# Kernel tuning notes

Hardware: AMD Instinct MI355X
Metric: run time of the kernel (lower is better)

The kernel has to match this reference:

```python
import jax, jax.numpy as jnp
import numpy as np

B, T, V, E, H, D = 2, 2048, 32000, 1024, 16, 64


def setup_inputs() -> dict:
    key = jax.random.key(0)
    ks = jax.random.split(key, 8)
    s = 0.02  # init scale
    return {
        "X": jax.random.randint(ks[0], (B, T), 0, V),
        "tok_emb": jax.random.normal(ks[1], (V, E), jnp.float32) * s,
        "pos_emb": jax.random.normal(ks[2], (T, E), jnp.float32) * s,
        "Wq": jax.random.normal(ks[3], (H, E, D), jnp.float32) * s,
        "Wk": jax.random.normal(ks[4], (H, E, D), jnp.float32) * s,
        "Wv": jax.random.normal(ks[5], (H, E, D), jnp.float32) * s,
        "lm_W": jax.random.normal(ks[6], (E, V), jnp.float32) * s,
        "lm_b": jnp.zeros((V,), jnp.float32),
    }


def reference(X, tok_emb, pos_emb, Wq, Wk, Wv, lm_W, lm_b):
    b, t = X.shape
    d = Wq.shape[-1]
    # token + position embedding
    x = tok_emb[X] + pos_emb[:t]  # [B,T,E]
    # per-head projections (stacked heads)
    q = jnp.einsum("bte,hed->bhtd", x, Wq)
    k = jnp.einsum("bte,hed->bhtd", x, Wk)
    v = jnp.einsum("bte,hed->bhtd", x, Wv)
    # causal attention, scale = head_size**-0.5
    scores = jnp.einsum("bhtd,bhsd->bhts", q, k) * (d ** -0.5)  # [B,H,T,T]
    mask = jnp.tril(jnp.ones((t, t), bool))
    scores = jnp.where(mask, scores, -jnp.inf)
    wei = jax.nn.softmax(scores, axis=-1)
    out = jnp.einsum("bhts,bhsd->bhtd", wei, v)
    out = out.transpose(0, 2, 1, 3).reshape(b, t, -1)  # concat heads -> [B,T,H*D]
    logits = out @ lm_W + lm_b  # [B,T,V]
    return logits
```

## Files before the change

kernel.cpp:

```cpp
#include <hip/hip_runtime.h>
#include <hip/hip_bf16.h>
#include <cstdint>

#define TSEQ 2048
#define NB   2
#define NH   16
#define EDIM 1024
#define DDIM 64
#define VOC  32000
#define MROWS (NB*TSEQ)
#define QKVN  (3*EDIM)

typedef _Float16 f16x8 __attribute__((ext_vector_type(8)));
typedef float    f32x4 __attribute__((ext_vector_type(4)));
typedef unsigned short u16x4v __attribute__((ext_vector_type(4)));
typedef unsigned short u16x8v __attribute__((ext_vector_type(8)));

__device__ __forceinline__ unsigned short f2h_bits(float v) {
  return __builtin_bit_cast(unsigned short, (_Float16)v);
}

__device__ __forceinline__ void gload_lds16(const void* g, void* l) {
  __builtin_amdgcn_global_load_lds((__attribute__((address_space(1))) void*)(g),
                                   (__attribute__((address_space(3))) void*)(l),
                                   16, 0, 0);
}

__global__ __launch_bounds__(256) void embed_kernel(
    const int* __restrict__ X, const float* __restrict__ tokE,
    const float* __restrict__ posE, unsigned short* __restrict__ x) {
  int g = blockIdx.x * 256 + threadIdx.x;
  int row = g >> 7;
  int e8  = (g & 127) * 8;
  int tk  = X[row];
  int tp  = row & (TSEQ - 1);
  const float4* ta = reinterpret_cast<const float4*>(&tokE[(size_t)tk * EDIM + e8]);
  const float4* pa = reinterpret_cast<const float4*>(&posE[(size_t)tp * EDIM + e8]);
  float4 a0 = ta[0], a1 = ta[1], p0 = pa[0], p1 = pa[1];
  u16x8v o;
  o[0] = f2h_bits(a0.x + p0.x); o[1] = f2h_bits(a0.y + p0.y);
  o[2] = f2h_bits(a0.z + p0.z); o[3] = f2h_bits(a0.w + p0.w);
  o[4] = f2h_bits(a1.x + p1.x); o[5] = f2h_bits(a1.y + p1.y);
  o[6] = f2h_bits(a1.z + p1.z); o[7] = f2h_bits(a1.w + p1.w);
  *reinterpret_cast<u16x8v*>(&x[(size_t)row * EDIM + e8]) = o;
}

__global__ __launch_bounds__(256) void trans_qkvw(
    const float* __restrict__ Wq, const float* __restrict__ Wk,
    const float* __restrict__ Wv, unsigned short* __restrict__ Wt) {
  __shared__ float ts[64][65];
  int bid = blockIdx.x;
  int mat = bid >> 8;
  int h   = (bid >> 4) & 15;
  int et  = bid & 15;
  const float* src = (mat == 0 ? Wq : (mat == 1 ? Wk : Wv)) + (size_t)h * EDIM * DDIM;
  int t = threadIdx.x;
  int rr = t >> 4, c4 = (t & 15) * 4;
#pragma unroll
  for (int p = 0; p < 4; ++p) {
    int r = p * 16 + rr;
    float4 v = *reinterpret_cast<const float4*>(&src[(size_t)(et * 64 + r) * DDIM + c4]);
    ts[r][c4 + 0] = v.x; ts[r][c4 + 1] = v.y; ts[r][c4 + 2] = v.z; ts[r][c4 + 3] = v.w;
  }
  __syncthreads();
#pragma unroll
  for (int p = 0; p < 4; ++p) {
    int dr = p * 16 + rr;
    u16x4v o;
#pragma unroll
    for (int j = 0; j < 4; ++j) o[j] = f2h_bits(ts[c4 + j][dr]);
    *reinterpret_cast<u16x4v*>(&Wt[((size_t)(mat * EDIM + h * 64 + dr)) * EDIM + et * 64 + c4]) = o;
  }
}

__global__ __launch_bounds__(256) void trans_lmw(
    const float* __restrict__ W, unsigned short* __restrict__ Wt) {
  __shared__ float ts[64][65];
  int bid = blockIdx.x;
  int vt = bid / 16, et = bid % 16;
  int t = threadIdx.x;
  int rr = t >> 4, c4 = (t & 15) * 4;
#pragma unroll
  for (int p = 0; p < 4; ++p) {
    int r = p * 16 + rr;
    float4 v = *reinterpret_cast<const float4*>(&W[(size_t)(et * 64 + r) * VOC + vt * 64 + c4]);
    ts[r][c4 + 0] = v.x; ts[r][c4 + 1] = v.y; ts[r][c4 + 2] = v.z; ts[r][c4 + 3] = v.w;
  }
  __syncthreads();
#pragma unroll
  for (int p = 0; p < 4; ++p) {
    int vr = p * 16 + rr;
    u16x4v o;
#pragma unroll
    for (int j = 0; j < 4; ++j) o[j] = f2h_bits(ts[c4 + j][vr]);
    *reinterpret_cast<u16x4v*>(&Wt[(size_t)(vt * 64 + vr) * EDIM + et * 64 + c4]) = o;
  }
}

template <bool F32OUT, bool BIAS>
__global__ __launch_bounds__(512, 4) void gemm128(
    const unsigned short* __restrict__ A, const unsigned short* __restrict__ Bt,
    float* __restrict__ Cf, unsigned short* __restrict__ Ch,
    const float* __restrict__ bias, int N, int K) {
  __shared__ __align__(16) unsigned short lds[3 * 12288];
  const int tid = threadIdx.x;
  const int w = tid >> 6, l = tid & 63;
  const int wr = w >> 2, wc = w & 3;
  const int l15 = l & 15, lhi = l >> 4;
  const int orig = blockIdx.x;
  const int bx = orig >> 5;
  const int by = orig & 31;
  const int m0 = by * 128, n0 = bx * 256;
  const int swzc = lhi ^ ((l15 >> 1) & 3);
  const int aOff = (wr * 64 + l15) * 32 + swzc * 8;
  const int bOff = 4096 + (wc * 64 + l15) * 32 + swzc * 8;
  const int sr = l >> 2;
  const int sc = (l & 3) ^ ((l >> 3) & 3);
  const unsigned short* PA = A  + (size_t)(m0 + w * 16 + sr) * K + sc * 8;
  const unsigned short* PB = Bt + (size_t)(n0 + w * 16 + sr) * K + sc * 8;
  const int dOff = w * 512;

#define STAGE32(ts, slot) do {                                                \
    gload_lds16(PA + (size_t)(ts) * 32, &lds[(slot) * 12288 + dOff]);         \
    gload_lds16(PB + (size_t)(ts) * 32, &lds[(slot) * 12288 + 4096 + dOff]);  \
    gload_lds16(PB + (size_t)128 * K + (size_t)(ts) * 32,                     \
                &lds[(slot) * 12288 + 8192 + dOff]);                          \
  } while (0)

  f32x4 acc[4][4] = {};
  STAGE32(0, 0);
  STAGE32(1, 1);
  asm volatile("s_waitcnt vmcnt(3)" ::: "memory");
  __builtin_amdgcn_sched_barrier(0);
  __builtin_amdgcn_s_barrier();

  const int NT = K >> 5;
  int slotC = 0;
  for (int t = 0; t < NT; ++t) {
    const int base = slotC * 12288;
    const int ts = (t + 2 < NT) ? (t + 2) : (NT - 1);
    int dslot = slotC + 2; if (dslot >= 3) dslot -= 3;
    STAGE32(ts, dslot);
    f16x8 bf[4];
#pragma unroll
    for (int q = 0; q < 4; ++q) bf[q] = *reinterpret_cast<const f16x8*>(&lds[base + bOff + q * 512]);
    f16x8 afq = *reinterpret_cast<const f16x8*>(&lds[base + aOff]);
    __builtin_amdgcn_s_setprio(1);
#pragma unroll
    for (int mi = 0; mi < 4; ++mi) {
      f16x8 afn = *reinterpret_cast<const f16x8*>(&lds[base + aOff + (((mi + 1) & 3)) * 512]);
#pragma unroll
      for (int ni = 0; ni < 4; ++ni)
        acc[mi][ni] = __builtin_amdgcn_mfma_f32_16x16x32_f16(afq, bf[ni], acc[mi][ni], 0, 0, 0);
      afq = afn;
    }
    __builtin_amdgcn_s_setprio(0);
    asm volatile("s_waitcnt vmcnt(3)" ::: "memory");
    __builtin_amdgcn_sched_barrier(0);
    __builtin_amdgcn_s_barrier();
    ++slotC; if (slotC == 3) slotC = 0;
  }
#undef STAGE32
  asm volatile("s_waitcnt vmcnt(0)" ::: "memory");

#pragma unroll
  for (int ni = 0; ni < 4; ++ni) {
    const int col = n0 + wc * 64 + ni * 16 + l15;
    float bv = BIAS ? bias[col] : 0.0f;
#pragma unroll
    for (int mi = 0; mi < 4; ++mi) {
#pragma unroll
      for (int r = 0; r < 4; ++r) {
        const size_t row = (size_t)m0 + wr * 64 + mi * 16 + lhi * 4 + r;
        float v = acc[mi][ni][r] + bv;
        if constexpr (F32OUT) __builtin_nontemporal_store(v, &Cf[row * (size_t)N + col]);
        else                  Ch[row * (size_t)N + col] = f2h_bits(v);
      }
    }
  }
}

template <bool F32OUT, bool BIAS>
__global__ __launch_bounds__(256, 2) void gemm128w(
    const unsigned short* __restrict__ A, const unsigned short* __restrict__ Bt,
    float* __restrict__ Cf, unsigned short* __restrict__ Ch,
    const float* __restrict__ bias, int N, int K) {
  __shared__ __align__(16) unsigned short lds[3 * 12288];
  const int tid = threadIdx.x;
  const int w = tid >> 6, l = tid & 63;
  const int l15 = l & 15, lhi = l >> 4;
  const int orig = blockIdx.x;
  const int bx = orig >> 5;
  const int by = orig & 31;
  const int m0 = by * 128, n0 = bx * 256;

  const int swzc = lhi ^ ((l15 >> 1) & 3);
  const int aOff = l15 * 32 + swzc * 8;
  const int bOff = 4096 + (w * 64 + l15) * 32 + swzc * 8;

  const int sr = l >> 2;
  const int sc = (l & 3) ^ ((l >> 3) & 3);
  const unsigned short* PA = A  + (size_t)(m0 + w * 16 + sr) * K + sc * 8;
  const unsigned short* PB = Bt + (size_t)(n0 + w * 64 + sr) * K + sc * 8;

#define STAGEW(ts, slot) do {                                                      \
    gload_lds16(PA + (size_t)(ts) * 32, &lds[(slot) * 12288 + w * 512]);           \
    gload_lds16(PA + (size_t)64 * K + (size_t)(ts) * 32,                           \
                &lds[(slot) * 12288 + 2048 + w * 512]);                            \
    gload_lds16(PB + (size_t)(ts) * 32,                                            \
                &lds[(slot) * 12288 + 4096 + w * 2048]);                           \
    gload_lds16(PB + (size_t)16 * K + (size_t)(ts) * 32,                           \
                &lds[(slot) * 12288 + 4096 + w * 2048 + 512]);                     \
    gload_lds16(PB + (size_t)32 * K + (size_t)(ts) * 32,                           \
                &lds[(slot) * 12288 + 4096 + w * 2048 + 1024]);                    \
    gload_lds16(PB + (size_t)48 * K + (size_t)(ts) * 32,                           \
                &lds[(slot) * 12288 + 4096 + w * 2048 + 1536]);                    \
  } while (0)

  f32x4 acc[8][4] = {};
  STAGEW(0, 0);
  STAGEW(1, 1);
  asm volatile("s_waitcnt vmcnt(6)" ::: "memory");
  __builtin_amdgcn_sched_barrier(0);
  __builtin_amdgcn_s_barrier();

  const int NT = K >> 5;
  int slotC = 0;
  for (int t = 0; t < NT; ++t) {
    const int base = slotC * 12288;
    const int ts = (t + 2 < NT) ? (t + 2) : (NT - 1);
    int dslot = slotC + 2; if (dslot >= 3) dslot -= 3;
    STAGEW(ts, dslot);
    f16x8 bf[4];
#pragma unroll
    for (int q = 0; q < 4; ++q) bf[q] = *reinterpret_cast<const f16x8*>(&lds[base + bOff + q * 512]);
    f16x8 afq = *reinterpret_cast<const f16x8*>(&lds[base + aOff]);
    __builtin_amdgcn_s_setprio(1);
#pragma unroll
    for (int mi = 0; mi < 8; ++mi) {
      f16x8 afn = *reinterpret_cast<const f16x8*>(&lds[base + aOff + (((mi + 1) & 7)) * 512]);
#pragma unroll
      for (int ni = 0; ni < 4; ++ni)
        acc[mi][ni] = __builtin_amdgcn_mfma_f32_16x16x32_f16(afq, bf[ni], acc[mi][ni], 0, 0, 0);
      afq = afn;
    }
    __builtin_amdgcn_s_setprio(0);
    asm volatile("s_waitcnt vmcnt(6)" ::: "memory");
    __builtin_amdgcn_sched_barrier(0);
    __builtin_amdgcn_s_barrier();
    ++slotC; if (slotC == 3) slotC = 0;
  }
#undef STAGEW
  asm volatile("s_waitcnt vmcnt(0)" ::: "memory");

#pragma unroll
  for (int ni = 0; ni < 4; ++ni) {
    const int col = n0 + w * 64 + ni * 16 + l15;
    float bv = BIAS ? bias[col] : 0.0f;
#pragma unroll
    for (int mi = 0; mi < 8; ++mi) {
#pragma unroll
      for (int r = 0; r < 4; ++r) {
        const size_t row = (size_t)m0 + mi * 16 + lhi * 4 + r;
        float v = acc[mi][ni][r] + bv;
        if constexpr (F32OUT) __builtin_nontemporal_store(v, &Cf[row * (size_t)N + col]);
        else                  Ch[row * (size_t)N + col] = f2h_bits(v);
      }
    }
  }
}

__global__ __launch_bounds__(256) void attn_kernel(
    const unsigned short* __restrict__ qkv, unsigned short* __restrict__ out) {
  __shared__ unsigned short Vt[2][64 * 72];
  __shared__ unsigned short Pl[4 * 16 * 72];
  const int bid = blockIdx.x;
  const int qt = bid & 31, bh = bid >> 5;
  const int b = bh >> 4, h = bh & 15;
  const int tid = threadIdx.x, w = tid >> 6, l = tid & 63;
  const int l15 = l & 15, lhi = l >> 4;
  const int q0 = qt * 64;
  const size_t RS = QKVN;
  const unsigned short* qbase = qkv + (size_t)b * TSEQ * RS + h * 64;
  const unsigned short* kbase = qbase + EDIM;
  const unsigned short* vbase = qbase + 2 * EDIM;

  f16x8 qa[2];
  {
    const int qrow = q0 + w * 16 + l15;
#pragma unroll
    for (int ks = 0; ks < 2; ++ks)
      qa[ks] = *reinterpret_cast<const f16x8*>(qbase + (size_t)qrow * RS + ks * 32 + lhi * 8);
  }
  const int vr_ = tid >> 3, vc8 = (tid & 7) * 8;
  {
#pragma unroll
    for (int p = 0; p < 2; ++p) {
      const int rr = vr_ + p * 32;
      u16x8v v = *reinterpret_cast<const u16x8v*>(vbase + (size_t)rr * RS + vc8);
#pragma unroll
      for (int j = 0; j < 8; ++j) Vt[0][(vc8 + j) * 72 + rr] = v[j];
    }
  }
  float m_run[4], l_run[4];
  f32x4 o[4] = {};
#pragma unroll
  for (int r = 0; r < 4; ++r) { m_run[r] = -__builtin_inff(); l_run[r] = 0.f; }
  const int myrow = q0 + w * 16 + lhi * 4;
  unsigned short* pl = &Pl[w * 16 * 72];
  __syncthreads();

  for (int kt = 0; kt <= qt; ++kt) {
    const int kv0 = kt * 64;
    const int tn = (kt + 1 <= qt) ? (kt + 1) : qt;
    u16x8v vpre[2];
#pragma unroll
    for (int p = 0; p < 2; ++p)
      vpre[p] = *reinterpret_cast<const u16x8v*>(
          vbase + (size_t)(tn * 64 + vr_ + p * 32) * RS + vc8);
    f32x4 s[4];
    __builtin_amdgcn_s_setprio(1);
#pragma unroll
    for (int ct = 0; ct < 4; ++ct) {
      f32x4 acc = {};
#pragma unroll
      for (int ks = 0; ks < 2; ++ks) {
        f16x8 kb = *reinterpret_cast<const f16x8*>(
            kbase + (size_t)(kv0 + ct * 16 + l15) * RS + ks * 32 + lhi * 8);
        acc = __builtin_amdgcn_mfma_f32_16x16x32_f16(qa[ks], kb, acc, 0, 0, 0);
      }
      s[ct] = acc;
    }
    __builtin_amdgcn_s_setprio(0);
    if (kt == qt) {
#pragma unroll
      for (int ct = 0; ct < 4; ++ct) {
        const int col = kv0 + ct * 16 + l15;
#pragma unroll
        for (int r = 0; r < 4; ++r) {
          float v = s[ct][r] * 0.125f;
          if (col > myrow + r) v = -__builtin_inff();
          s[ct][r] = v;
        }
      }
    } else {
#pragma unroll
      for (int ct = 0; ct < 4; ++ct)
#pragma unroll
        for (int r = 0; r < 4; ++r) s[ct][r] *= 0.125f;
    }
    float alpha[4];
#pragma unroll
    for (int r = 0; r < 4; ++r) {
      float mx = fmaxf(fmaxf(s[0][r], s[1][r]), fmaxf(s[2][r], s[3][r]));
      mx = fmaxf(mx, __shfl_xor(mx, 1)); mx = fmaxf(mx, __shfl_xor(mx, 2));
      mx = fmaxf(mx, __shfl_xor(mx, 4)); mx = fmaxf(mx, __shfl_xor(mx, 8));
      const float mn = fmaxf(m_run[r], mx);
      alpha[r] = __expf(m_run[r] - mn);
      m_run[r] = mn;
    }
    float rs[4] = {0.f, 0.f, 0.f, 0.f};
#pragma unroll
    for (int ct = 0; ct < 4; ++ct)
#pragma unroll
      for (int r = 0; r < 4; ++r) {
        const float p = __expf(s[ct][r] - m_run[r]);
        s[ct][r] = p;
        rs[r] += p;
      }
#pragma unroll
    for (int r = 0; r < 4; ++r) {
      float t = rs[r];
      t += __shfl_xor(t, 1); t += __shfl_xor(t, 2);
      t += __shfl_xor(t, 4); t += __shfl_xor(t, 8);
      l_run[r] = l_run[r] * alpha[r] + t;
    }
#pragma unroll
    for (int ct = 0; ct < 4; ++ct)
#pragma unroll
      for (int r = 0; r < 4; ++r) o[ct][r] *= alpha[r];
#pragma unroll
    for (int ct = 0; ct < 4; ++ct)
#pragma unroll
      for (int r = 0; r < 4; ++r)
        pl[(lhi * 4 + r) * 72 + ct * 16 + l15] = f2h_bits(s[ct][r]);
    const unsigned short* vt = Vt[kt & 1];
#pragma unroll
    for (int ks = 0; ks < 2; ++ks) {
      f16x8 pa = *reinterpret_cast<const f16x8*>(&pl[l15 * 72 + ks * 32 + lhi * 8]);
      __builtin_amdgcn_s_setprio(1);
#pragma unroll
      for (int ct = 0; ct < 4; ++ct) {
        f16x8 vb = *reinterpret_cast<const f16x8*>(&vt[(ct * 16 + l15) * 72 + ks * 32 + lhi * 8]);
        o[ct] = __builtin_amdgcn_mfma_f32_16x16x32_f16(pa, vb, o[ct], 0, 0, 0);
      }
      __builtin_amdgcn_s_setprio(0);
    }
    if (kt < qt) {
      unsigned short* vtn = Vt[(kt + 1) & 1];
#pragma unroll
      for (int p = 0; p < 2; ++p) {
        const int rr = vr_ + p * 32;
#pragma unroll
        for (int j = 0; j < 8; ++j) vtn[(vc8 + j) * 72 + rr] = vpre[p][j];
      }
    }
    __syncthreads();
  }
  unsigned short* obase = out + ((size_t)(b * TSEQ + q0 + w * 16)) * EDIM + h * 64;
#pragma unroll
  for (int r = 0; r < 4; ++r) {
    const float linv = 1.0f / l_run[r];
#pragma unroll
    for (int ct = 0; ct < 4; ++ct) {
      obase[(size_t)(lhi * 4 + r) * EDIM + ct * 16 + l15] = f2h_bits(o[ct][r] * linv);
    }
  }
}

extern "C" void kernel_launch(void* const* d_in, const int* in_sizes, int n_in,
                              void* d_out, int out_size, void* d_ws, size_t ws_size,
                              hipStream_t stream) {
  const int*   X    = (const int*)d_in[0];
  const float* tokE = (const float*)d_in[1];
  const float* posE = (const float*)d_in[2];
  const float* Wq   = (const float*)d_in[3];
  const float* Wk   = (const float*)d_in[4];
  const float* Wv   = (const float*)d_in[5];
  const float* lmW  = (const float*)d_in[6];
  const float* lmb  = (const float*)d_in[7];
  float* out = (float*)d_out;

  unsigned short* ws   = (unsigned short*)d_ws;
  unsigned short* x    = ws;
  unsigned short* att  = x    + (size_t)MROWS * EDIM;
  unsigned short* wqkv = att  + (size_t)MROWS * EDIM;
  unsigned short* qkv  = wqkv + (size_t)QKVN * EDIM;
  unsigned short* lmWt = qkv  + (size_t)MROWS * QKVN;

  embed_kernel<<<(MROWS * EDIM / 8) / 256, 256, 0, stream>>>(X, tokE, posE, x);
  trans_qkvw<<<3 * NH * (EDIM / 64), 256, 0, stream>>>(Wq, Wk, Wv, wqkv);
  trans_lmw<<<(VOC / 64) * (EDIM / 64), 256, 0, stream>>>(lmW, lmWt);
  gemm128<false, false><<<(QKVN / 256) * (MROWS / 128), 512, 0, stream>>>(
      x, wqkv, nullptr, qkv, nullptr, QKVN, EDIM);
  attn_kernel<<<NB * NH * (TSEQ / 64), 256, 0, stream>>>(qkv, att);
  gemm128w<true, true><<<(VOC / 256) * (MROWS / 128), 256, 0, stream>>>(
      att, lmWt, out, nullptr, lmb, VOC, EDIM);
}
```

Before: 523.1 us.

## Load LM-head B tiles directly into registers, keep only A in LDS

In the LM-head GEMM, each wave now reads its own 64-column B fragments straight from global memory into registers. These are double-buffered across K steps with an unrolled two-step loop. Only the A tile is still staged through the triple-buffered LDS ring, which shrinks LDS use from 72KB to 24KB per block. Because each wave uses its B slice exclusively, the LDS round-trip and ds_read traffic for B are removed. In exchange, the global-load latency for B is exposed directly in registers, coalescing is less regular, and register pressure goes up.

After: 621.8 us. 1.19x slower.

```diff
diff --git a/kernel.cpp b/kernel.cpp
--- a/kernel.cpp
+++ b/kernel.cpp
@@ -181,11 +181,11 @@
 }
 
 template <bool F32OUT, bool BIAS>
-__global__ __launch_bounds__(256, 2) void gemm128w(
+__global__ __launch_bounds__(256, 2) void gemm128d(
     const unsigned short* __restrict__ A, const unsigned short* __restrict__ Bt,
     float* __restrict__ Cf, unsigned short* __restrict__ Ch,
     const float* __restrict__ bias, int N, int K) {
-  __shared__ __align__(16) unsigned short lds[3 * 12288];
+  __shared__ __align__(16) unsigned short lds[3 * 4096];
   const int tid = threadIdx.x;
   const int w = tid >> 6, l = tid & 63;
   const int l15 = l & 15, lhi = l >> 4;
@@ -196,61 +196,84 @@
 
   const int swzc = lhi ^ ((l15 >> 1) & 3);
   const int aOff = l15 * 32 + swzc * 8;
-  const int bOff = 4096 + (w * 64 + l15) * 32 + swzc * 8;
 
   const int sr = l >> 2;
   const int sc = (l & 3) ^ ((l >> 3) & 3);
-  const unsigned short* PA = A  + (size_t)(m0 + w * 16 + sr) * K + sc * 8;
-  const unsigned short* PB = Bt + (size_t)(n0 + w * 64 + sr) * K + sc * 8;
-
-#define STAGEW(ts, slot) do {                                                      \
-    gload_lds16(PA + (size_t)(ts) * 32, &lds[(slot) * 12288 + w * 512]);           \
-    gload_lds16(PA + (size_t)64 * K + (size_t)(ts) * 32,                           \
-                &lds[(slot) * 12288 + 2048 + w * 512]);                            \
-    gload_lds16(PB + (size_t)(ts) * 32,                                            \
-                &lds[(slot) * 12288 + 4096 + w * 2048]);                           \
-    gload_lds16(PB + (size_t)16 * K + (size_t)(ts) * 32,                           \
-                &lds[(slot) * 12288 + 4096 + w * 2048 + 512]);                     \
-    gload_lds16(PB + (size_t)32 * K + (size_t)(ts) * 32,                           \
-                &lds[(slot) * 12288 + 4096 + w * 2048 + 1024]);                    \
-    gload_lds16(PB + (size_t)48 * K + (size_t)(ts) * 32,                           \
-                &lds[(slot) * 12288 + 4096 + w * 2048 + 1536]);                    \
+  const unsigned short* PA = A + (size_t)(m0 + w * 16 + sr) * K + sc * 8;
+
+  const unsigned short* BF = Bt + (size_t)(n0 + w * 64 + l15) * K + lhi * 8;
+
+#define STAGEA(ts, slot) do {                                                 \
+    gload_lds16(PA + (size_t)(ts) * 32, &lds[(slot) * 4096 + w * 512]);       \
+    gload_lds16(PA + (size_t)64 * K + (size_t)(ts) * 32,                      \
+                &lds[(slot) * 4096 + 2048 + w * 512]);                        \
   } while (0)
 
   f32x4 acc[8][4] = {};
-  STAGEW(0, 0);
-  STAGEW(1, 1);
-  asm volatile("s_waitcnt vmcnt(6)" ::: "memory");
+  f16x8 b0[4], b1[4];
+  STAGEA(0, 0);
+  STAGEA(1, 1);
+#pragma unroll
+  for (int q = 0; q < 4; ++q)
+    b0[q] = *reinterpret_cast<const f16x8*>(BF + (size_t)q * 16 * K);
+  asm volatile("s_waitcnt vmcnt(2)" ::: "memory");
   __builtin_amdgcn_sched_barrier(0);
   __builtin_amdgcn_s_barrier();
 
   const int NT = K >> 5;
   int slotC = 0;
-  for (int t = 0; t < NT; ++t) {
-    const int base = slotC * 12288;
-    const int ts = (t + 2 < NT) ? (t + 2) : (NT - 1);
-    int dslot = slotC + 2; if (dslot >= 3) dslot -= 3;
-    STAGEW(ts, dslot);
-    f16x8 bf[4];
-#pragma unroll
-    for (int q = 0; q < 4; ++q) bf[q] = *reinterpret_cast<const f16x8*>(&lds[base + bOff + q * 512]);
-    f16x8 afq = *reinterpret_cast<const f16x8*>(&lds[base + aOff]);
-    __builtin_amdgcn_s_setprio(1);
-#pragma unroll
-    for (int mi = 0; mi < 8; ++mi) {
-      f16x8 afn = *reinterpret_cast<const f16x8*>(&lds[base + aOff + (((mi + 1) & 7)) * 512]);
-#pragma unroll
-      for (int ni = 0; ni < 4; ++ni)
-        acc[mi][ni] = __builtin_amdgcn_mfma_f32_16x16x32_f16(afq, bf[ni], acc[mi][ni], 0, 0, 0);
-      afq = afn;
-    }
-    __builtin_amdgcn_s_setprio(0);
-    asm volatile("s_waitcnt vmcnt(6)" ::: "memory");
-    __builtin_amdgcn_sched_barrier(0);
-    __builtin_amdgcn_s_barrier();
-    ++slotC; if (slotC == 3) slotC = 0;
-  }
-#undef STAGEW
+  for (int t = 0; t < NT; t += 2) {
+    {
+      const int base = slotC * 4096;
+      const int ts = (t + 2 < NT) ? (t + 2) : (NT - 1);
+      int dslot = slotC + 2; if (dslot >= 3) dslot -= 3;
+#pragma unroll
+      for (int q = 0; q < 4; ++q)
+        b1[q] = *reinterpret_cast<const f16x8*>(BF + (size_t)q * 16 * K + (size_t)(t + 1) * 32);
+      STAGEA(ts, dslot);
+      f16x8 afq = *reinterpret_cast<const f16x8*>(&lds[base + aOff]);
+      __builtin_amdgcn_s_setprio(1);
+#pragma unroll
+      for (int mi = 0; mi < 8; ++mi) {
+        f16x8 afn = *reinterpret_cast<const f16x8*>(&lds[base + aOff + (((mi + 1) & 7)) * 512]);
+#pragma unroll
+        for (int ni = 0; ni < 4; ++ni)
+          acc[mi][ni] = __builtin_amdgcn_mfma_f32_16x16x32_f16(afq, b0[ni], acc[mi][ni], 0, 0, 0);
+        afq = afn;
+      }
+      __builtin_amdgcn_s_setprio(0);
+      asm volatile("s_waitcnt vmcnt(6)" ::: "memory");
+      __builtin_amdgcn_sched_barrier(0);
+      __builtin_amdgcn_s_barrier();
+      ++slotC; if (slotC == 3) slotC = 0;
+    }
+    {
+      const int base = slotC * 4096;
+      const int tb = (t + 2 < NT) ? (t + 2) : (NT - 1);
+      const int ts = (t + 3 < NT) ? (t + 3) : (NT - 1);
+      int dslot = slotC + 2; if (dslot >= 3) dslot -= 3;
+#pragma unroll
+      for (int q = 0; q < 4; ++q)
+        b0[q] = *reinterpret_cast<const f16x8*>(BF + (size_t)q * 16 * K + (size_t)tb * 32);
+      STAGEA(ts, dslot);
+      f16x8 afq = *reinterpret_cast<const f16x8*>(&lds[base + aOff]);
+      __builtin_amdgcn_s_setprio(1);
+#pragma unroll
+      for (int mi = 0; mi < 8; ++mi) {
+        f16x8 afn = *reinterpret_cast<const f16x8*>(&lds[base + aOff + (((mi + 1) & 7)) * 512]);
+#pragma unroll
+        for (int ni = 0; ni < 4; ++ni)
+          acc[mi][ni] = __builtin_amdgcn_mfma_f32_16x16x32_f16(afq, b1[ni], acc[mi][ni], 0, 0, 0);
+        afq = afn;
+      }
+      __builtin_amdgcn_s_setprio(0);
+      asm volatile("s_waitcnt vmcnt(6)" ::: "memory");
+      __builtin_amdgcn_sched_barrier(0);
+      __builtin_amdgcn_s_barrier();
+      ++slotC; if (slotC == 3) slotC = 0;
+    }
+  }
+#undef STAGEA
   asm volatile("s_waitcnt vmcnt(0)" ::: "memory");
 
 #pragma unroll
@@ -444,6 +467,6 @@
   gemm128<false, false><<<(QKVN / 256) * (MROWS / 128), 512, 0, stream>>>(
       x, wqkv, nullptr, qkv, nullptr, QKVN, EDIM);
   attn_kernel<<<NB * NH * (TSEQ / 64), 256, 0, stream>>>(qkv, att);
-  gemm128w<true, true><<<(VOC / 256) * (MROWS / 128), 256, 0, stream>>>(
+  gemm128d<true, true><<<(VOC / 256) * (MROWS / 128), 256, 0, stream>>>(
       att, lmWt, out, nullptr, lmb, VOC, EDIM);
 }
```

## Use 128-row query tiles with 8 waves per attention block

Applied to the files above, without the earlier changes.

The attention kernel now handles 128 query rows per block using 512 threads (8 waves), which halves the number of blocks and lets one shared V tile in LDS serve twice as many query rows. Each thread now loads one V row chunk instead of two. Waves whose rows lie entirely before a key tile skip its compute but still join the barrier and the V staging. The cost is lower grid parallelism (512 blocks) and idle waves on the diagonal tiles.

New measurement: 544.0 us. +4.0%, slower.

```diff
diff --git a/kernel.cpp b/kernel.cpp
--- a/kernel.cpp
+++ b/kernel.cpp
@@ -270,16 +270,17 @@
   }
 }
 
-__global__ __launch_bounds__(256) void attn_kernel(
+__global__ __launch_bounds__(512) void attn_kernel(
     const unsigned short* __restrict__ qkv, unsigned short* __restrict__ out) {
   __shared__ unsigned short Vt[2][64 * 72];
-  __shared__ unsigned short Pl[4 * 16 * 72];
+  __shared__ unsigned short Pl[8 * 16 * 72];
   const int bid = blockIdx.x;
-  const int qt = bid & 31, bh = bid >> 5;
+  const int qt = bid & 15, bh = bid >> 4;
   const int b = bh >> 4, h = bh & 15;
   const int tid = threadIdx.x, w = tid >> 6, l = tid & 63;
   const int l15 = l & 15, lhi = l >> 4;
-  const int q0 = qt * 64;
+  const int q0 = qt * 128;
+  const int wrow = q0 + w * 16;
   const size_t RS = QKVN;
   const unsigned short* qbase = qkv + (size_t)b * TSEQ * RS + h * 64;
   const unsigned short* kbase = qbase + EDIM;
@@ -287,127 +288,119 @@
 
   f16x8 qa[2];
   {
-    const int qrow = q0 + w * 16 + l15;
+    const int qrow = wrow + l15;
 #pragma unroll
     for (int ks = 0; ks < 2; ++ks)
       qa[ks] = *reinterpret_cast<const f16x8*>(qbase + (size_t)qrow * RS + ks * 32 + lhi * 8);
   }
   const int vr_ = tid >> 3, vc8 = (tid & 7) * 8;
   {
-#pragma unroll
-    for (int p = 0; p < 2; ++p) {
-      const int rr = vr_ + p * 32;
-      u16x8v v = *reinterpret_cast<const u16x8v*>(vbase + (size_t)rr * RS + vc8);
-#pragma unroll
-      for (int j = 0; j < 8; ++j) Vt[0][(vc8 + j) * 72 + rr] = v[j];
-    }
+    u16x8v v = *reinterpret_cast<const u16x8v*>(vbase + (size_t)vr_ * RS + vc8);
+#pragma unroll
+    for (int j = 0; j < 8; ++j) Vt[0][(vc8 + j) * 72 + vr_] = v[j];
   }
   float m_run[4], l_run[4];
   f32x4 o[4] = {};
 #pragma unroll
   for (int r = 0; r < 4; ++r) { m_run[r] = -__builtin_inff(); l_run[r] = 0.f; }
-  const int myrow = q0 + w * 16 + lhi * 4;
+  const int myrow = wrow + lhi * 4;
   unsigned short* pl = &Pl[w * 16 * 72];
   __syncthreads();
 
-  for (int kt = 0; kt <= qt; ++kt) {
+  const int nkt = 2 * qt + 2;
+  for (int kt = 0; kt < nkt; ++kt) {
     const int kv0 = kt * 64;
-    const int tn = (kt + 1 <= qt) ? (kt + 1) : qt;
-    u16x8v vpre[2];
-#pragma unroll
-    for (int p = 0; p < 2; ++p)
-      vpre[p] = *reinterpret_cast<const u16x8v*>(
-          vbase + (size_t)(tn * 64 + vr_ + p * 32) * RS + vc8);
-    f32x4 s[4];
-    __builtin_amdgcn_s_setprio(1);
-#pragma unroll
-    for (int ct = 0; ct < 4; ++ct) {
-      f32x4 acc = {};
+    const int tn = (kt + 1 < nkt) ? (kt + 1) : kt;
+    u16x8v vpre = *reinterpret_cast<const u16x8v*>(
+        vbase + (size_t)(tn * 64 + vr_) * RS + vc8);
+    if (kv0 <= wrow + 15) {
+      f32x4 s[4];
+      __builtin_amdgcn_s_setprio(1);
+#pragma unroll
+      for (int ct = 0; ct < 4; ++ct) {
+        f32x4 acc = {};
+#pragma unroll
+        for (int ks = 0; ks < 2; ++ks) {
+          f16x8 kb = *reinterpret_cast<const f16x8*>(
+              kbase + (size_t)(kv0 + ct * 16 + l15) * RS + ks * 32 + lhi * 8);
+          acc = __builtin_amdgcn_mfma_f32_16x16x32_f16(qa[ks], kb, acc, 0, 0, 0);
+        }
+        s[ct] = acc;
+      }
+      __builtin_amdgcn_s_setprio(0);
+      if (kv0 + 63 > wrow) {
+#pragma unroll
+        for (int ct = 0; ct < 4; ++ct) {
+          const int col = kv0 + ct * 16 + l15;
+#pragma unroll
+          for (int r = 0; r < 4; ++r) {
+            float v = s[ct][r] * 0.125f;
+            if (col > myrow + r) v = -__builtin_inff();
+            s[ct][r] = v;
+          }
+        }
+      } else {
+#pragma unroll
+        for (int ct = 0; ct < 4; ++ct)
+#pragma unroll
+          for (int r = 0; r < 4; ++r) s[ct][r] *= 0.125f;
+      }
+      float alpha[4];
+#pragma unroll
+      for (int r = 0; r < 4; ++r) {
+        float mx = fmaxf(fmaxf(s[0][r], s[1][r]), fmaxf(s[2][r], s[3][r]));
+        mx = fmaxf(mx, __shfl_xor(mx, 1)); mx = fmaxf(mx, __shfl_xor(mx, 2));
+        mx = fmaxf(mx, __shfl_xor(mx, 4)); mx = fmaxf(mx, __shfl_xor(mx, 8));
+        const float mn = fmaxf(m_run[r], mx);
+        alpha[r] = __expf(m_run[r] - mn);
+        m_run[r] = mn;
+      }
+      float rs[4] = {0.f, 0.f, 0.f, 0.f};
+#pragma unroll
+      for (int ct = 0; ct < 4; ++ct)
+#pragma unroll
+        for (int r = 0; r < 4; ++r) {
+          const float p = __expf(s[ct][r] - m_run[r]);
+          s[ct][r] = p;
+          rs[r] += p;
+        }
+#pragma unroll
+      for (int r = 0; r < 4; ++r) {
+        float t = rs[r];
+        t += __shfl_xor(t, 1); t += __shfl_xor(t, 2);
+        t += __shfl_xor(t, 4); t += __shfl_xor(t, 8);
+        l_run[r] = l_run[r] * alpha[r] + t;
+      }
+#pragma unroll
+      for (int ct = 0; ct < 4; ++ct)
+#pragma unroll
+        for (int r = 0; r < 4; ++r) o[ct][r] *= alpha[r];
+#pragma unroll
+      for (int ct = 0; ct < 4; ++ct)
+#pragma unroll
+        for (int r = 0; r < 4; ++r)
+          pl[(lhi * 4 + r) * 72 + ct * 16 + l15] = f2h_bits(s[ct][r]);
+      const unsigned short* vt = Vt[kt & 1];
 #pragma unroll
       for (int ks = 0; ks < 2; ++ks) {
-        f16x8 kb = *reinterpret_cast<const f16x8*>(
-            kbase + (size_t)(kv0 + ct * 16 + l15) * RS + ks * 32 + lhi * 8);
-        acc = __builtin_amdgcn_mfma_f32_16x16x32_f16(qa[ks], kb, acc, 0, 0, 0);
-      }
-      s[ct] = acc;
-    }
-    __builtin_amdgcn_s_setprio(0);
-    if (kt == qt) {
-#pragma unroll
-      for (int ct = 0; ct < 4; ++ct) {
-        const int col = kv0 + ct * 16 + l15;
-#pragma unroll
-        for (int r = 0; r < 4; ++r) {
-          float v = s[ct][r] * 0.125f;
-          if (col > myrow + r) v = -__builtin_inff();
-          s[ct][r] = v;
+        f16x8 pa = *reinterpret_cast<const f16x8*>(&pl[l15 * 72 + ks * 32 + lhi * 8]);
+        __builtin_amdgcn_s_setprio(1);
+#pragma unroll
+        for (int ct = 0; ct < 4; ++ct) {
+          f16x8 vb = *reinterpret_cast<const f16x8*>(&vt[(ct * 16 + l15) * 72 + ks * 32 + lhi * 8]);
+          o[ct] = __builtin_amdgcn_mfma_f32_16x16x32_f16(pa, vb, o[ct], 0, 0, 0);
         }
-      }
-    } else {
-#pragma unroll
-      for (int ct = 0; ct < 4; ++ct)
-#pragma unroll
-        for (int r = 0; r < 4; ++r) s[ct][r] *= 0.125f;
-    }
-    float alpha[4];
-#pragma unroll
-    for (int r = 0; r < 4; ++r) {
-      float mx = fmaxf(fmaxf(s[0][r], s[1][r]), fmaxf(s[2][r], s[3][r]));
-      mx = fmaxf(mx, __shfl_xor(mx, 1)); mx = fmaxf(mx, __shfl_xor(mx, 2));
-      mx = fmaxf(mx, __shfl_xor(mx, 4)); mx = fmaxf(mx, __shfl_xor(mx, 8));
-      const float mn = fmaxf(m_run[r], mx);
-      alpha[r] = __expf(m_run[r] - mn);
-      m_run[r] = mn;
-    }
-    float rs[4] = {0.f, 0.f, 0.f, 0.f};
-#pragma unroll
-    for (int ct = 0; ct < 4; ++ct)
-#pragma unroll
-      for (int r = 0; r < 4; ++r) {
-        const float p = __expf(s[ct][r] - m_run[r]);
-        s[ct][r] = p;
-        rs[r] += p;
-      }
-#pragma unroll
-    for (int r = 0; r < 4; ++r) {
-      float t = rs[r];
-      t += __shfl_xor(t, 1); t += __shfl_xor(t, 2);
-      t += __shfl_xor(t, 4); t += __shfl_xor(t, 8);
-      l_run[r] = l_run[r] * alpha[r] + t;
-    }
-#pragma unroll
-    for (int ct = 0; ct < 4; ++ct)
-#pragma unroll
-      for (int r = 0; r < 4; ++r) o[ct][r] *= alpha[r];
-#pragma unroll
-    for (int ct = 0; ct < 4; ++ct)
-#pragma unroll
-      for (int r = 0; r < 4; ++r)
-        pl[(lhi * 4 + r) * 72 + ct * 16 + l15] = f2h_bits(s[ct][r]);
-    const unsigned short* vt = Vt[kt & 1];
-#pragma unroll
-    for (int ks = 0; ks < 2; ++ks) {
-      f16x8 pa = *reinterpret_cast<const f16x8*>(&pl[l15 * 72 + ks * 32 + lhi * 8]);
-      __builtin_amdgcn_s_setprio(1);
-#pragma unroll
-      for (int ct = 0; ct < 4; ++ct) {
-        f16x8 vb = *reinterpret_cast<const f16x8*>(&vt[(ct * 16 + l15) * 72 + ks * 32 + lhi * 8]);
-        o[ct] = __builtin_amdgcn_mfma_f32_16x16x32_f16(pa, vb, o[ct], 0, 0, 0);
-      }
-      __builtin_amdgcn_s_setprio(0);
-    }
-    if (kt < qt) {
+        __builtin_amdgcn_s_setprio(0);
+      }
+    }
+    if (kt + 1 < nkt) {
       unsigned short* vtn = Vt[(kt + 1) & 1];
 #pragma unroll
-      for (int p = 0; p < 2; ++p) {
-        const int rr = vr_ + p * 32;
-#pragma unroll
-        for (int j = 0; j < 8; ++j) vtn[(vc8 + j) * 72 + rr] = vpre[p][j];
-      }
+      for (int j = 0; j < 8; ++j) vtn[(vc8 + j) * 72 + vr_] = vpre[j];
     }
     __syncthreads();
   }
-  unsigned short* obase = out + ((size_t)(b * TSEQ + q0 + w * 16)) * EDIM + h * 64;
+  unsigned short* obase = out + ((size_t)(b * TSEQ + wrow)) * EDIM + h * 64;
 #pragma unroll
   for (int r = 0; r < 4; ++r) {
     const float linv = 1.0f / l_run[r];
@@ -443,7 +436,7 @@
   trans_lmw<<<(VOC / 64) * (EDIM / 64), 256, 0, stream>>>(lmW, lmWt);
   gemm128<false, false><<<(QKVN / 256) * (MROWS / 128), 512, 0, stream>>>(
       x, wqkv, nullptr, qkv, nullptr, QKVN, EDIM);
-  attn_kernel<<<NB * NH * (TSEQ / 64), 256, 0, stream>>>(qkv, att);
+  attn_kernel<<<NB * NH * (TSEQ / 128), 512, 0, stream>>>(qkv, att);
   gemm128w<true, true><<<(VOC / 256) * (MROWS / 128), 256, 0, stream>>>(
       att, lmWt, out, nullptr, lmb, VOC, EDIM);
 }
```
